# Optimization experiments

Measured on AMD Instinct MI355X. Metric: run time of the kernel, lower is better.

## Reference

```python
import jax, jax.numpy as jnp
import numpy as np

HEADS = 16

def setup_inputs() -> dict:
    key = jax.random.key(0)
    ks = jax.random.split(key, 5)
    B, T, D = 2, 2048, 2048
    s = 0.02
    return {
        "x": jax.random.normal(ks[0], (B, T, D), dtype=jnp.float32),
        "Wq": jax.random.normal(ks[1], (D, D), dtype=jnp.float32) * s,
        "Wk": jax.random.normal(ks[2], (D, D), dtype=jnp.float32) * s,
        "Wv": jax.random.normal(ks[3], (D, D), dtype=jnp.float32) * s,
        "Wo": jax.random.normal(ks[4], (D, D), dtype=jnp.float32) * s,
    }

def reference(x, Wq, Wk, Wv, Wo):
    B, T, _ = x.shape
    H = HEADS
    Dh = Wq.shape[1] // H
    # projections: [B,T,H,Dh]
    q = (x @ Wq).reshape(B, T, H, Dh)
    k = (x @ Wk).reshape(B, T, H, Dh)
    v = (x @ Wv).reshape(B, T, H, Dh)
    # raw scores [B,H,T,T]
    scores = jnp.einsum("bthd,bshd->bhts", q, k)
    # NOTE (faithful to source): mask is multiplicative 0/1 tril (the
    # masked_fill(-inf) in the torch code is not in-place and has no effect),
    # and the scale is sqrt(token_len), not sqrt(head_dim).
    mask = jnp.tril(jnp.ones((T, T), dtype=scores.dtype))
    scores = scores * mask
    attn = jax.nn.softmax(scores / (T ** 0.5), axis=-1)
    out = jnp.einsum("bhts,bshd->bthd", attn, v).reshape(B, T, H * Dh)
    return out @ Wo
```

## Files before the change

kernel.cpp:

```cpp
#include <hip/hip_runtime.h>


typedef __attribute__((ext_vector_type(4))) float  f32x4;
typedef __attribute__((ext_vector_type(8))) short  bf16x8;
typedef __attribute__((ext_vector_type(4))) unsigned short u16x4;

#define AS1 __attribute__((address_space(1)))
#define AS3 __attribute__((address_space(3)))

__device__ __forceinline__ void llds16(const void* g, void* l) {
  __builtin_amdgcn_global_load_lds((const AS1 void*)g, (AS3 void*)l, 16, 0, 0);
}

__device__ __forceinline__ unsigned short f2bf(float f) {
  unsigned int u = __builtin_bit_cast(unsigned int, f);
  u += 0x7fffu + ((u >> 16) & 1u);
  return (unsigned short)(u >> 16);
}

__device__ __forceinline__ unsigned short f2bfru(float f) {
  return (unsigned short)((__builtin_bit_cast(unsigned int, f) + 0x8000u) >> 16);
}

__device__ __forceinline__ float bf2f(unsigned short u) {
  return __builtin_bit_cast(float, (unsigned int)u << 16);
}

__global__ __launch_bounds__(256) void cast_x_kernel(const float* __restrict__ in,
                                                     unsigned short* __restrict__ out) {
  int i = blockIdx.x * 256 + threadIdx.x;
  f32x4 v = ((const f32x4*)in)[i];
  u16x4 o;
  o[0] = f2bf(v[0]); o[1] = f2bf(v[1]); o[2] = f2bf(v[2]); o[3] = f2bf(v[3]);
  ((u16x4*)out)[i] = o;
}

__global__ __launch_bounds__(256) void transpose_w4_kernel(
    const float* __restrict__ W0, const float* __restrict__ W1,
    const float* __restrict__ W2, const float* __restrict__ W3,
    unsigned short* __restrict__ T0, unsigned short* __restrict__ T1,
    unsigned short* __restrict__ T2, unsigned short* __restrict__ T3) {
  __shared__ float tile[32][33];
  const int z = blockIdx.z;
  const float* W = (z == 0) ? W0 : (z == 1) ? W1 : (z == 2) ? W2 : W3;
  unsigned short* Wt = (z == 0) ? T0 : (z == 1) ? T1 : (z == 2) ? T2 : T3;
  const int bx = blockIdx.x << 5;
  const int by = blockIdx.y << 5;
  const int tx = threadIdx.x;
  const int ty = threadIdx.y;
#pragma unroll
  for (int r = ty; r < 32; r += 8)
    tile[r][tx] = W[(size_t)(bx + r) * 2048 + by + tx];
  __syncthreads();
#pragma unroll
  for (int r = ty; r < 32; r += 8)
    Wt[(size_t)(by + r) * 2048 + bx + tx] = f2bf(tile[tx][r]);
}

template <int EPI>
__global__ __launch_bounds__(256, 2) void gemm_pipe(const unsigned short* __restrict__ A,
                                                    const unsigned short* __restrict__ Bt,
                                                    unsigned short* __restrict__ Qb,
                                                    unsigned short* __restrict__ Kb,
                                                    unsigned short* __restrict__ Vt,
                                                    float* __restrict__ Co) {
  constexpr int BN      = (EPI == 0) ? 256 : 128;
  constexpr int MI      = (EPI == 0) ? 8 : 4;
  constexpr int BROUNDS = BN / 64;
  constexpr int SLOT    = 8192 + BN * 64;
  __shared__ __align__(16) char smem[3 * SLOT];

  const int tid  = threadIdx.x;
  const int lane = tid & 63;
  const int w    = tid >> 6;
  const int q16  = lane >> 4;
  const int l15  = lane & 15;
  const int f    = blockIdx.x;
  const int g    = f >> 3;
  int bm, bn;
  if constexpr (EPI == 0) { bn = (f & 7) * 3 + (g % 3); bm = g / 3; }
  else                    { bn = ((f & 7) << 1) + (g & 1); bm = g >> 1; }
  const int wmb = (EPI == 0) ? 0 : ((w >> 1) << 6);
  const int wnb = (EPI == 0) ? (w << 6) : ((w & 1) << 6);

  f32x4 acc[MI][4];
#pragma unroll
  for (int i = 0; i < MI; ++i)
#pragma unroll
    for (int j = 0; j < 4; ++j) acc[i][j] = (f32x4){0.f, 0.f, 0.f, 0.f};

  const int rowA = tid >> 2;
  const int chA  = tid & 3;
  auto stageT = [&](int t, char* sb) {
    const int k0 = t << 5;
#pragma unroll
    for (int r = 0; r < 2; ++r) {
      int row = (r << 6) + rowA;
      const unsigned short* src = A + (size_t)((bm << 7) + row) * 2048 + k0
                                    + ((chA ^ ((row >> 1) & 3)) << 3);
      llds16(src, sb + (r << 12) + (w << 10));
    }
#pragma unroll
    for (int r = 0; r < BROUNDS; ++r) {
      int row = (r << 6) + rowA;
      const unsigned short* src = Bt + (size_t)(bn * BN + row) * 2048 + k0
                                     + ((chA ^ ((row >> 1) & 3)) << 3);
      llds16(src, sb + 8192 + (r << 12) + (w << 10));
    }
  };

  auto computeT = [&](const char* base) {
    bf16x8 af[MI], bf[4];
#pragma unroll
    for (int mi = 0; mi < MI; ++mi) {
      int row = wmb + (mi << 4) + l15;
      af[mi] = *(const bf16x8*)(base + (row << 6) + ((q16 ^ ((row >> 1) & 3)) << 4));
    }
#pragma unroll
    for (int ni = 0; ni < 4; ++ni) {
      int row = wnb + (ni << 4) + l15;
      bf[ni] = *(const bf16x8*)(base + 8192 + (row << 6) + ((q16 ^ ((row >> 1) & 3)) << 4));
    }
    __builtin_amdgcn_s_setprio(1);
#pragma unroll
    for (int mi = 0; mi < MI; ++mi)
#pragma unroll
      for (int ni = 0; ni < 4; ++ni)
        acc[mi][ni] = __builtin_amdgcn_mfma_f32_16x16x32_bf16(af[mi], bf[ni], acc[mi][ni], 0, 0, 0);
    __builtin_amdgcn_s_setprio(0);
  };

  auto WAITC = [&]() {
    if constexpr (EPI == 0) asm volatile("s_waitcnt vmcnt(6)" ::: "memory");
    else                    asm volatile("s_waitcnt vmcnt(4)" ::: "memory");
  };
  auto STEP = [&](int t, char* cbase, char* sbase) {
    WAITC();
    __builtin_amdgcn_s_barrier();
    stageT(t + 2, sbase);
    computeT(cbase);
  };

  char* s0 = smem;
  char* s1 = smem + SLOT;
  char* s2 = smem + 2 * SLOT;

  stageT(0, s0); stageT(1, s1);

#pragma unroll 1
  for (int t = 0; t < 60; t += 3) {
    STEP(t,     s0, s2);
    STEP(t + 1, s1, s0);
    STEP(t + 2, s2, s1);
  }
  STEP(60, s0, s2);
  STEP(61, s1, s0);
  WAITC();
  __builtin_amdgcn_s_barrier();
  computeT(s2);
  asm volatile("s_waitcnt vmcnt(0)" ::: "memory");
  __builtin_amdgcn_s_barrier();
  computeT(s0);

  const float qscale = 0.02209708691207961f;
  const int rb = q16 << 2;
#pragma unroll
  for (int mi = 0; mi < MI; ++mi) {
    int m0 = (bm << 7) + wmb + (mi << 4) + rb;
#pragma unroll
    for (int ni = 0; ni < 4; ++ni) {
      if constexpr (EPI == 0) {
        int region = bn >> 3;
        int nloc = ((bn & 7) << 8) + wnb + (ni << 4) + l15;
        if (region == 0) {
#pragma unroll
          for (int j = 0; j < 4; ++j)
            Qb[(size_t)(m0 + j) * 2048 + nloc] = f2bf(acc[mi][ni][j] * qscale);
        } else if (region == 1) {
#pragma unroll
          for (int j = 0; j < 4; ++j)
            Kb[(size_t)(m0 + j) * 2048 + nloc] = f2bf(acc[mi][ni][j]);
        } else {
          u16x4 pk;
#pragma unroll
          for (int j = 0; j < 4; ++j) pk[j] = f2bf(acc[mi][ni][j]);
          int b = m0 >> 11, t = m0 & 2047;
          *(u16x4*)(Vt + ((size_t)((b << 4) + (nloc >> 7)) * 128 + (nloc & 127)) * 2048 + t) = pk;
        }
      } else {
        int n = (bn << 7) + wnb + (ni << 4) + l15;
#pragma unroll
        for (int j = 0; j < 4; ++j)
          Co[(size_t)(m0 + j) * 2048 + n] = acc[mi][ni][j];
      }
    }
  }
}

__global__ __launch_bounds__(256) void vsuf_kernel(const unsigned short* __restrict__ Vt,
                                                   float* __restrict__ Suf) {
  const int row  = blockIdx.x * 4 + (threadIdx.x >> 6);
  const int lane = threadIdx.x & 63;
  const unsigned short* vp = Vt + (size_t)row * 2048 + (lane << 5);
  float a = 0.f;
#pragma unroll
  for (int c = 0; c < 4; ++c) {
    bf16x8 v = *(const bf16x8*)(vp + (c << 3));
#pragma unroll
    for (int j = 0; j < 8; ++j) a += bf2f((unsigned short)v[j]);
  }
  float I = a;
#pragma unroll
  for (int off = 1; off < 64; off <<= 1) {
    float t = __shfl_down(I, off, 64);
    I += (lane + off < 64) ? t : 0.f;
  }
  Suf[(size_t)lane * 4096 + row] = I;
  if (lane == 0) Suf[(size_t)64 * 4096 + row] = 0.f;
}

__global__ __launch_bounds__(256) void attn_kernel(const unsigned short* __restrict__ Q,
                                                   const unsigned short* __restrict__ K,
                                                   const unsigned short* __restrict__ V,
                                                   const float* __restrict__ Suf,
                                                   unsigned short* __restrict__ O) {
  __shared__ __align__(16) char smem[36864];
  const int tid  = threadIdx.x;
  const int lane = tid & 63;
  const int w    = tid >> 6;
  const int q16  = lane >> 4;
  const int l15  = lane & 15;
  const int f    = blockIdx.x;
  const int bh    = ((f & 7) << 2) + ((f >> 3) & 3);
  const int strip = 31 - (f >> 5);
  const int b  = bh >> 4;
  const size_t qkbase = ((size_t)(b << 11)) * 2048 + ((size_t)(bh & 15) << 7);
  const size_t vbase  = (size_t)bh << 18;
  const int rb = q16 << 2;
  char* Psm = smem + 32768 + (w << 10);

  const int numIter = 2 * strip + 2;
  const int t0 = (strip << 6) + (w << 4);

  auto stage = [&](int s0, int kb, int vb) {
#pragma unroll
    for (int c = 0; c < 2; ++c) {
      int ch = (w << 1) + c;
      int rowK = (ch << 2) + q16;
      int colbK = (l15 << 4) ^ ((rowK & 7) << 4);
      llds16(K + qkbase + (size_t)(s0 + rowK) * 2048 + (colbK >> 1), smem + kb + (ch << 10));
      int rowV = (ch << 4) + (lane >> 2);
      int colbV = ((lane & 3) << 4) ^ (((rowV >> 2) & 3) << 4);
      llds16(V + vbase + (size_t)rowV * 2048 + s0 + (colbV >> 1), smem + vb + (ch << 10));
    }
  };

  bf16x8 qf[4];
  {
    const unsigned short* qp = Q + qkbase + (size_t)(t0 + l15) * 2048 + (q16 << 3);
#pragma unroll
    for (int kk = 0; kk < 4; ++kk) qf[kk] = *(const bf16x8*)(qp + (kk << 5));
  }

  f32x4 oacc[8];
#pragma unroll
  for (int i = 0; i < 8; ++i) oacc[i] = (f32x4){0.f, 0.f, 0.f, 0.f};
  float ell[4] = {0.f, 0.f, 0.f, 0.f};

  stage(0, 0, 16384);
  asm volatile("s_waitcnt vmcnt(0)" ::: "memory");
  __syncthreads();

  int cur = 0;
  for (int it = 0; it < numIter; ++it) {
    const int s0 = it << 5;
    if (it + 1 < numIter)
      stage(s0 + 32, (cur ^ 1) << 13, 16384 + ((cur ^ 1) << 13));

    if (s0 <= t0) {
      const int kb = cur << 13;
      const int vb = 16384 + (cur << 13);

      f32x4 sA = (f32x4){0.f, 0.f, 0.f, 0.f}, sB = (f32x4){0.f, 0.f, 0.f, 0.f};
#pragma unroll
      for (int kk = 0; kk < 4; ++kk) {
        int r0 = l15;
        bf16x8 k0f = *(const bf16x8*)(smem + kb + (r0 << 8) + (((kk << 6) + (q16 << 4)) ^ ((r0 & 7) << 4)));
        sA = __builtin_amdgcn_mfma_f32_16x16x32_bf16(qf[kk], k0f, sA, 0, 0, 0);
        int r1 = 16 + l15;
        bf16x8 k1f = *(const bf16x8*)(smem + kb + (r1 << 8) + (((kk << 6) + (q16 << 4)) ^ ((r1 & 7) << 4)));
        sB = __builtin_amdgcn_mfma_f32_16x16x32_bf16(qf[kk], k1f, sB, 0, 0, 0);
      }

      float pA[4], pB[4];
      if (s0 + 31 <= t0) {
#pragma unroll
        for (int j = 0; j < 4; ++j) {
          pA[j] = __expf(sA[j]);
          pB[j] = __expf(sB[j]);
          ell[j] += pA[j] + pB[j];
        }
      } else {
#pragma unroll
        for (int j = 0; j < 4; ++j) {
          int t  = t0 + rb + j;
          int sa = s0 + l15;
          float vA = (sa <= t)      ? sA[j] : 0.f;
          float vB = (sa + 16 <= t) ? sB[j] : 0.f;
          pA[j] = __expf(vA);
          pB[j] = __expf(vB);
          ell[j] += pA[j] + pB[j];
        }
      }

#pragma unroll
      for (int j = 0; j < 4; ++j) {
        int r   = rb + j;
        int swz = ((r >> 1) & 3) << 4;
        *(unsigned short*)(Psm + (r << 6) + ((l15 << 1) ^ swz))        = f2bfru(pA[j]);
        *(unsigned short*)(Psm + (r << 6) + ((32 + (l15 << 1)) ^ swz)) = f2bfru(pB[j]);
      }
      asm volatile("s_waitcnt lgkmcnt(0)" ::: "memory");

      bf16x8 pa;
      {
        int r = l15;
        pa = *(const bf16x8*)(Psm + (r << 6) + ((q16 << 4) ^ (((r >> 1) & 3) << 4)));
      }
#pragma unroll
      for (int ni = 0; ni < 8; ++ni) {
        int dr = (ni << 4) + l15;
        bf16x8 vbf = *(const bf16x8*)(smem + vb + (dr << 6) + ((q16 << 4) ^ (((dr >> 2) & 3) << 4)));
        oacc[ni] = __builtin_amdgcn_mfma_f32_16x16x32_bf16(pa, vbf, oacc[ni], 0, 0, 0);
      }
    }

    asm volatile("s_waitcnt vmcnt(0)" ::: "memory");
    __syncthreads();
    cur ^= 1;
  }

  const int send = (t0 & ~31) + 32;
  const float* sp = Suf + (size_t)(send >> 5) * 4096 + ((size_t)bh << 7);
  const float extra = (float)(2048 - send);
#pragma unroll
  for (int ni = 0; ni < 8; ++ni) {
    float sv = sp[(ni << 4) + l15];
#pragma unroll
    for (int j = 0; j < 4; ++j) oacc[ni][j] += sv;
  }

#pragma unroll
  for (int j = 0; j < 4; ++j) {
    float r = ell[j];
    r += __shfl_xor(r, 1, 64);
    r += __shfl_xor(r, 2, 64);
    r += __shfl_xor(r, 4, 64);
    r += __shfl_xor(r, 8, 64);
    float inv = 1.0f / (r + extra);
    int t = t0 + rb + j;
    unsigned short* op = O + qkbase + (size_t)t * 2048;
#pragma unroll
    for (int ni = 0; ni < 8; ++ni)
      op[(ni << 4) + l15] = f2bf(oacc[ni][j] * inv);
  }
}

extern "C" void kernel_launch(void* const* d_in, const int* in_sizes, int n_in,
                              void* d_out, int out_size, void* d_ws, size_t ws_size,
                              hipStream_t stream) {
  (void)in_sizes; (void)n_in; (void)out_size; (void)ws_size;
  const float* x  = (const float*)d_in[0];
  const float* Wq = (const float*)d_in[1];
  const float* Wk = (const float*)d_in[2];
  const float* Wv = (const float*)d_in[3];
  const float* Wo = (const float*)d_in[4];
  float* out = (float*)d_out;

  char* ws = (char*)d_ws;
  unsigned short* Xb  = (unsigned short*)(ws);
  unsigned short* Wqt = (unsigned short*)(ws + 16777216);
  unsigned short* Wkt = (unsigned short*)(ws + 16777216 + 8388608);
  unsigned short* Wvt = (unsigned short*)(ws + 16777216 + 2 * 8388608);
  unsigned short* Wot = (unsigned short*)(ws + 16777216 + 3 * 8388608);
  unsigned short* Qb  = (unsigned short*)(ws + 50331648);
  unsigned short* Kb  = (unsigned short*)(ws + 67108864);
  unsigned short* Vt  = (unsigned short*)(ws + 83886080);
  unsigned short* Ob  = Xb;
  float*          Suf = (float*)Wqt;

  cast_x_kernel<<<8192, 256, 0, stream>>>(x, Xb);
  {
    dim3 tb(32, 8), tg(64, 64, 4);
    transpose_w4_kernel<<<tg, tb, 0, stream>>>(Wq, Wk, Wv, Wo, Wqt, Wkt, Wvt, Wot);
  }
  gemm_pipe<0><<<768, 256, 0, stream>>>(Xb, Wqt, Qb, Kb, Vt, nullptr);

  vsuf_kernel<<<1024, 256, 0, stream>>>(Vt, Suf);

  attn_kernel<<<1024, 256, 0, stream>>>(Qb, Kb, Vt, Suf, Ob);

  gemm_pipe<1><<<512, 256, 0, stream>>>(Ob, Wot, nullptr, nullptr, nullptr, out);
}
```

Measured before the change: 261.6 us.

## Replace QKV GEMM with 8-wave 128x384 tile, BK=64 double-buffered kernel

Splits the templated GEMM into a dedicated QKV kernel and a Wo kernel. The QKV projection now uses 512-thread blocks computing 128x384 output tiles with a 64-wide K step. It double-buffers 64KB LDS slots and interleaves LDS reads, global-to-LDS loads and MFMA bursts across barriers in a ping-pong schedule. This aims for higher arithmetic intensity per block and better overlap of loads with matrix math than the previous 128x256, three-stage, 256-thread design. In exchange it uses 128KB of LDS per block, which limits occupancy, and adds many barriers per K tile.

Result: no change. 257.0 us (-1.8%).

```diff
diff --git a/kernel.cpp b/kernel.cpp
--- a/kernel.cpp
+++ b/kernel.cpp
@@ -57,17 +57,164 @@
     Wt[(size_t)(by + r) * 2048 + bx + tx] = f2bf(tile[tx][r]);
 }
 
-template <int EPI>
-__global__ __launch_bounds__(256, 2) void gemm_pipe(const unsigned short* __restrict__ A,
+__global__ __launch_bounds__(512, 2) void gemm_qkv8(const unsigned short* __restrict__ A,
                                                     const unsigned short* __restrict__ Bt,
                                                     unsigned short* __restrict__ Qb,
                                                     unsigned short* __restrict__ Kb,
-                                                    unsigned short* __restrict__ Vt,
-                                                    float* __restrict__ Co) {
-  constexpr int BN      = (EPI == 0) ? 256 : 128;
-  constexpr int MI      = (EPI == 0) ? 8 : 4;
-  constexpr int BROUNDS = BN / 64;
-  constexpr int SLOT    = 8192 + BN * 64;
+                                                    unsigned short* __restrict__ Vt) {
+  __shared__ __align__(16) char smem[131072];
+  const int tid  = threadIdx.x;
+  const int lane = tid & 63;
+  const int w    = tid >> 6;
+  const int wr   = w >> 2;
+  const int wc   = w & 3;
+  const int q16  = lane >> 4;
+  const int l15  = lane & 15;
+  const int f    = blockIdx.x;
+  const int bn   = ((f & 7) << 1) + ((f >> 3) & 1);
+  const int bm   = f >> 4;
+
+  const int srow = tid >> 3;
+  const int scl  = (tid & 7) ^ (srow & 7);
+  const unsigned short* aS = A  + (size_t)((bm << 7) + srow) * 2048 + (scl << 3);
+  const unsigned short* bS = Bt + (size_t)(bn * 384 + srow) * 2048 + (scl << 3);
+  const int sdst = tid << 4;
+
+  const int swzb = (q16 ^ (l15 & 7)) << 4;
+  const int aRd  = ((wr << 6) + l15) << 7;
+  const int bRd  = 16384 + ((wc * 96 + l15) << 7);
+
+  f32x4 acc[4][6];
+#pragma unroll
+  for (int i = 0; i < 4; ++i)
+#pragma unroll
+    for (int j = 0; j < 6; ++j) acc[i][j] = (f32x4){0.f, 0.f, 0.f, 0.f};
+
+  bf16x8 af[4], bf[3];
+
+  auto TILE = [&](int kt, int cb, int ob, bool st) {
+    const int kn = (kt + 1) << 6;
+#pragma unroll
+    for (int mi = 0; mi < 4; ++mi)
+      af[mi] = *(const bf16x8*)(smem + cb + aRd + (mi << 11) + swzb);
+#pragma unroll
+    for (int r = 0; r < 3; ++r)
+      bf[r] = *(const bf16x8*)(smem + cb + bRd + (r << 11) + swzb);
+    if (st) {
+      llds16(aS + kn,              smem + ob + sdst);
+      llds16(aS + (1 << 17) + kn,  smem + ob + 8192 + sdst);
+      llds16(bS + kn,              smem + ob + 16384 + sdst);
+    }
+    asm volatile("s_barrier" ::: "memory");
+    __builtin_amdgcn_s_setprio(1);
+#pragma unroll
+    for (int mi = 0; mi < 4; ++mi)
+#pragma unroll
+      for (int r = 0; r < 3; ++r)
+        acc[mi][r] = __builtin_amdgcn_mfma_f32_16x16x32_bf16(af[mi], bf[r], acc[mi][r], 0, 0, 0);
+    __builtin_amdgcn_s_setprio(0);
+    asm volatile("s_barrier" ::: "memory");
+#pragma unroll
+    for (int r = 0; r < 3; ++r)
+      bf[r] = *(const bf16x8*)(smem + cb + bRd + ((3 + r) << 11) + swzb);
+    if (st) {
+      llds16(bS + (1 << 17) + kn,  smem + ob + 16384 + 8192 + sdst);
+      llds16(bS + (2 << 17) + kn,  smem + ob + 16384 + 16384 + sdst);
+      llds16(bS + (3 << 17) + kn,  smem + ob + 16384 + 24576 + sdst);
+    }
+    asm volatile("s_barrier" ::: "memory");
+    __builtin_amdgcn_s_setprio(1);
+#pragma unroll
+    for (int mi = 0; mi < 4; ++mi)
+#pragma unroll
+      for (int r = 0; r < 3; ++r)
+        acc[mi][3 + r] = __builtin_amdgcn_mfma_f32_16x16x32_bf16(af[mi], bf[r], acc[mi][3 + r], 0, 0, 0);
+    __builtin_amdgcn_s_setprio(0);
+    asm volatile("s_barrier" ::: "memory");
+#pragma unroll
+    for (int mi = 0; mi < 4; ++mi)
+      af[mi] = *(const bf16x8*)(smem + cb + aRd + (mi << 11) + (swzb ^ 64));
+#pragma unroll
+    for (int r = 0; r < 3; ++r)
+      bf[r] = *(const bf16x8*)(smem + cb + bRd + (r << 11) + (swzb ^ 64));
+    if (st) {
+      llds16(bS + (4 << 17) + kn,  smem + ob + 16384 + 32768 + sdst);
+      llds16(bS + (5 << 17) + kn,  smem + ob + 16384 + 40960 + sdst);
+    }
+    asm volatile("s_barrier" ::: "memory");
+    __builtin_amdgcn_s_setprio(1);
+#pragma unroll
+    for (int mi = 0; mi < 4; ++mi)
+#pragma unroll
+      for (int r = 0; r < 3; ++r)
+        acc[mi][r] = __builtin_amdgcn_mfma_f32_16x16x32_bf16(af[mi], bf[r], acc[mi][r], 0, 0, 0);
+    __builtin_amdgcn_s_setprio(0);
+    asm volatile("s_barrier" ::: "memory");
+#pragma unroll
+    for (int r = 0; r < 3; ++r)
+      bf[r] = *(const bf16x8*)(smem + cb + bRd + ((3 + r) << 11) + (swzb ^ 64));
+    asm volatile("s_barrier" ::: "memory");
+    __builtin_amdgcn_s_setprio(1);
+#pragma unroll
+    for (int mi = 0; mi < 4; ++mi)
+#pragma unroll
+      for (int r = 0; r < 3; ++r)
+        acc[mi][3 + r] = __builtin_amdgcn_mfma_f32_16x16x32_bf16(af[mi], bf[r], acc[mi][3 + r], 0, 0, 0);
+    __builtin_amdgcn_s_setprio(0);
+    asm volatile("s_barrier" ::: "memory");
+    asm volatile("s_waitcnt vmcnt(0)" ::: "memory");
+    asm volatile("s_barrier" ::: "memory");
+  };
+
+  llds16(aS, smem + sdst);
+  llds16(aS + (1 << 17), smem + 8192 + sdst);
+#pragma unroll
+  for (int li = 0; li < 6; ++li)
+    llds16(bS + li * (1 << 17), smem + 16384 + li * 8192 + sdst);
+  asm volatile("s_waitcnt vmcnt(0)" ::: "memory");
+  asm volatile("s_barrier" ::: "memory");
+
+#pragma unroll 1
+  for (int kt = 0; kt < 30; kt += 2) {
+    TILE(kt,     0,     65536, true);
+    TILE(kt + 1, 65536, 0,     true);
+  }
+  TILE(30, 0,     65536, true);
+  TILE(31, 65536, 0,     false);
+
+  const float qscale = 0.02209708691207961f;
+  const int rb = q16 << 2;
+#pragma unroll
+  for (int mi = 0; mi < 4; ++mi) {
+    int m0 = (bm << 7) + (wr << 6) + (mi << 4) + rb;
+#pragma unroll
+    for (int ni = 0; ni < 6; ++ni) {
+      int gn = bn * 384 + wc * 96 + (ni << 4) + l15;
+      int region = gn >> 11;
+      int nloc = gn & 2047;
+      if (region == 0) {
+#pragma unroll
+        for (int j = 0; j < 4; ++j)
+          Qb[(size_t)(m0 + j) * 2048 + nloc] = f2bf(acc[mi][ni][j] * qscale);
+      } else if (region == 1) {
+#pragma unroll
+        for (int j = 0; j < 4; ++j)
+          Kb[(size_t)(m0 + j) * 2048 + nloc] = f2bf(acc[mi][ni][j]);
+      } else {
+        u16x4 pk;
+#pragma unroll
+        for (int j = 0; j < 4; ++j) pk[j] = f2bf(acc[mi][ni][j]);
+        int b = m0 >> 11, t = m0 & 2047;
+        *(u16x4*)(Vt + ((size_t)((b << 4) + (nloc >> 7)) * 128 + (nloc & 127)) * 2048 + t) = pk;
+      }
+    }
+  }
+}
+
+__global__ __launch_bounds__(256, 2) void gemm_wo(const unsigned short* __restrict__ A,
+                                                  const unsigned short* __restrict__ Bt,
+                                                  float* __restrict__ Co) {
+  constexpr int SLOT = 8192 + 8192;
   __shared__ __align__(16) char smem[3 * SLOT];
 
   const int tid  = threadIdx.x;
@@ -77,15 +224,14 @@
   const int l15  = lane & 15;
   const int f    = blockIdx.x;
   const int g    = f >> 3;
-  int bm, bn;
-  if constexpr (EPI == 0) { bn = (f & 7) * 3 + (g % 3); bm = g / 3; }
-  else                    { bn = ((f & 7) << 1) + (g & 1); bm = g >> 1; }
-  const int wmb = (EPI == 0) ? 0 : ((w >> 1) << 6);
-  const int wnb = (EPI == 0) ? (w << 6) : ((w & 1) << 6);
-
-  f32x4 acc[MI][4];
-#pragma unroll
-  for (int i = 0; i < MI; ++i)
+  const int bn   = ((f & 7) << 1) + (g & 1);
+  const int bm   = g >> 1;
+  const int wmb  = (w >> 1) << 6;
+  const int wnb  = (w & 1) << 6;
+
+  f32x4 acc[4][4];
+#pragma unroll
+  for (int i = 0; i < 4; ++i)
 #pragma unroll
     for (int j = 0; j < 4; ++j) acc[i][j] = (f32x4){0.f, 0.f, 0.f, 0.f};
 
@@ -101,18 +247,18 @@
       llds16(src, sb + (r << 12) + (w << 10));
     }
 #pragma unroll
-    for (int r = 0; r < BROUNDS; ++r) {
+    for (int r = 0; r < 2; ++r) {
       int row = (r << 6) + rowA;
-      const unsigned short* src = Bt + (size_t)(bn * BN + row) * 2048 + k0
+      const unsigned short* src = Bt + (size_t)((bn << 7) + row) * 2048 + k0
                                      + ((chA ^ ((row >> 1) & 3)) << 3);
       llds16(src, sb + 8192 + (r << 12) + (w << 10));
     }
   };
 
   auto computeT = [&](const char* base) {
-    bf16x8 af[MI], bf[4];
-#pragma unroll
-    for (int mi = 0; mi < MI; ++mi) {
+    bf16x8 af[4], bf[4];
+#pragma unroll
+    for (int mi = 0; mi < 4; ++mi) {
       int row = wmb + (mi << 4) + l15;
       af[mi] = *(const bf16x8*)(base + (row << 6) + ((q16 ^ ((row >> 1) & 3)) << 4));
     }
@@ -123,19 +269,15 @@
     }
     __builtin_amdgcn_s_setprio(1);
 #pragma unroll
-    for (int mi = 0; mi < MI; ++mi)
+    for (int mi = 0; mi < 4; ++mi)
 #pragma unroll
       for (int ni = 0; ni < 4; ++ni)
         acc[mi][ni] = __builtin_amdgcn_mfma_f32_16x16x32_bf16(af[mi], bf[ni], acc[mi][ni], 0, 0, 0);
     __builtin_amdgcn_s_setprio(0);
   };
 
-  auto WAITC = [&]() {
-    if constexpr (EPI == 0) asm volatile("s_waitcnt vmcnt(6)" ::: "memory");
-    else                    asm volatile("s_waitcnt vmcnt(4)" ::: "memory");
-  };
   auto STEP = [&](int t, char* cbase, char* sbase) {
-    WAITC();
+    asm volatile("s_waitcnt vmcnt(4)" ::: "memory");
     __builtin_amdgcn_s_barrier();
     stageT(t + 2, sbase);
     computeT(cbase);
@@ -146,7 +288,6 @@
   char* s2 = smem + 2 * SLOT;
 
   stageT(0, s0); stageT(1, s1);
-
 #pragma unroll 1
   for (int t = 0; t < 60; t += 3) {
     STEP(t,     s0, s2);
@@ -155,44 +296,23 @@
   }
   STEP(60, s0, s2);
   STEP(61, s1, s0);
-  WAITC();
+  asm volatile("s_waitcnt vmcnt(4)" ::: "memory");
   __builtin_amdgcn_s_barrier();
   computeT(s2);
   asm volatile("s_waitcnt vmcnt(0)" ::: "memory");
   __builtin_amdgcn_s_barrier();
   computeT(s0);
 
-  const float qscale = 0.02209708691207961f;
   const int rb = q16 << 2;
 #pragma unroll
-  for (int mi = 0; mi < MI; ++mi) {
+  for (int mi = 0; mi < 4; ++mi) {
     int m0 = (bm << 7) + wmb + (mi << 4) + rb;
 #pragma unroll
     for (int ni = 0; ni < 4; ++ni) {
-      if constexpr (EPI == 0) {
-        int region = bn >> 3;
-        int nloc = ((bn & 7) << 8) + wnb + (ni << 4) + l15;
-        if (region == 0) {
-#pragma unroll
-          for (int j = 0; j < 4; ++j)
-            Qb[(size_t)(m0 + j) * 2048 + nloc] = f2bf(acc[mi][ni][j] * qscale);
-        } else if (region == 1) {
-#pragma unroll
-          for (int j = 0; j < 4; ++j)
-            Kb[(size_t)(m0 + j) * 2048 + nloc] = f2bf(acc[mi][ni][j]);
-        } else {
-          u16x4 pk;
-#pragma unroll
-          for (int j = 0; j < 4; ++j) pk[j] = f2bf(acc[mi][ni][j]);
-          int b = m0 >> 11, t = m0 & 2047;
-          *(u16x4*)(Vt + ((size_t)((b << 4) + (nloc >> 7)) * 128 + (nloc & 127)) * 2048 + t) = pk;
-        }
-      } else {
-        int n = (bn << 7) + wnb + (ni << 4) + l15;
-#pragma unroll
-        for (int j = 0; j < 4; ++j)
-          Co[(size_t)(m0 + j) * 2048 + n] = acc[mi][ni][j];
-      }
+      int n = (bn << 7) + wnb + (ni << 4) + l15;
+#pragma unroll
+      for (int j = 0; j < 4; ++j)
+        Co[(size_t)(m0 + j) * 2048 + n] = acc[mi][ni][j];
     }
   }
 }
@@ -394,11 +514,11 @@
     dim3 tb(32, 8), tg(64, 64, 4);
     transpose_w4_kernel<<<tg, tb, 0, stream>>>(Wq, Wk, Wv, Wo, Wqt, Wkt, Wvt, Wot);
   }
-  gemm_pipe<0><<<768, 256, 0, stream>>>(Xb, Wqt, Qb, Kb, Vt, nullptr);
+  gemm_qkv8<<<512, 512, 0, stream>>>(Xb, Wqt, Qb, Kb, Vt);
 
   vsuf_kernel<<<1024, 256, 0, stream>>>(Vt, Suf);
 
   attn_kernel<<<1024, 256, 0, stream>>>(Qb, Kb, Vt, Suf, Ob);
 
-  gemm_pipe<1><<<512, 256, 0, stream>>>(Ob, Wot, nullptr, nullptr, nullptr, out);
-}
+  gemm_wo<<<512, 256, 0, stream>>>(Ob, Wot, out);
+}
```
